# Performance work log

Measured on AMD Instinct MI355X. Metric: run time of the kernel, lower is better.

The kernel has to match this reference:

```python
import jax, jax.numpy as jnp
import numpy as np

N = 100000
E = 600000
IN_DIM = 128
HID = 128


def setup_inputs() -> dict:
    key = jax.random.key(0)
    ks = jax.random.split(key, 12)
    def lin(kw, fan_in, fan_out):
        # torch nn.Linear default init: U(-1/sqrt(fan_in), 1/sqrt(fan_in))
        bound = 1.0 / np.sqrt(fan_in)
        kw1, kw2 = jax.random.split(kw)
        w = jax.random.uniform(kw1, (fan_in, fan_out), jnp.float32, -bound, bound)
        b = jax.random.uniform(kw2, (fan_out,), jnp.float32, -bound, bound)
        return w, b
    x = jax.random.normal(ks[0], (N, IN_DIM), jnp.float32)
    edge_index = jax.random.randint(ks[1], (2, E), 0, N, jnp.int64)
    w1a, b1a = lin(ks[2], IN_DIM, HID)
    w1b, b1b = lin(ks[3], HID, HID)
    w2a, b2a = lin(ks[4], HID, HID)
    w2b, b2b = lin(ks[5], HID, HID)
    wo, bo = lin(ks[6], HID, 1)
    return {"x": x, "edge_index": edge_index,
            "w1a": w1a, "b1a": b1a, "w1b": w1b, "b1b": b1b,
            "w2a": w2a, "b2a": b2a, "w2b": w2b, "b2b": b2b,
            "wo": wo, "bo": bo}


def _gin_conv(x, src, dst, wa, ba, wb, bb):
    # sum-aggregate neighbor features: agg[dst] += x[src]; eps = 0 (GIN default)
    agg = jax.ops.segment_sum(x[src], dst, num_segments=N)
    h = x + agg
    h = jax.nn.relu(h @ wa + ba)
    return h @ wb + bb


def reference(x, edge_index, w1a, b1a, w1b, b1b, w2a, b2a, w2b, b2b, wo, bo):
    src, dst = edge_index[0], edge_index[1]
    h = _gin_conv(x, src, dst, w1a, b1a, w1b, b1b)
    h = _gin_conv(h, src, dst, w2a, b2a, w2b, b2b)
    return (h @ wo + bo).squeeze(-1)  # [N]
```

## Files before the change

### kernel.cpp

```cpp
#include <hip/hip_runtime.h>

typedef unsigned short u16;
typedef unsigned int u32;
typedef __bf16 bf16x8 __attribute__((ext_vector_type(8)));
typedef float f32x4 __attribute__((ext_vector_type(4)));

#define CAP 32

__device__ __forceinline__ u16 f2bf(float f) {
  union { float f; u32 u; } c; c.f = f;
  return (u16)((c.u + 0x7fffu + ((c.u >> 16) & 1u)) >> 16);
}
__device__ __forceinline__ float2 upk2(u32 v) {
  union { u32 u; float f; } a, b; a.u = v << 16; b.u = v & 0xffff0000u;
  return make_float2(a.f, b.f);
}
__device__ __forceinline__ u32 pk2(float x, float y) {
  return (u32)f2bf(x) | ((u32)f2bf(y) << 16);
}

__global__ __launch_bounds__(256) void k_prep2(const float4* __restrict__ x4,
                                               uint2* __restrict__ xb,
                                               int n4, int castBlocks, int trBlocks,
                                               const float* __restrict__ w0,
                                               const float* __restrict__ w1,
                                               const float* __restrict__ w2,
                                               const float* __restrict__ w3,
                                               u16* __restrict__ wT,
                                               int* __restrict__ cursor, int N) {
  int b = blockIdx.x, t = threadIdx.x;
  if (b < castBlocks) {
    int i = b * 256 + t;
    if (i < n4) {
      float4 v = x4[i];
      xb[i] = make_uint2(pk2(v.x, v.y), pk2(v.z, v.w));
    }
  } else if (b < castBlocks + trBlocks) {
    int id = (b - castBlocks) * 256 + t;
    int w = id >> 14, rem = id & 16383;
    int nn = rem >> 7, kk = rem & 127;
    const float* s = (w == 0) ? w0 : (w == 1) ? w1 : (w == 2) ? w2 : w3;
    wT[id] = f2bf(s[kk * 128 + nn]);
  } else {
    int i = (b - castBlocks - trBlocks) * 256 + t;
    if (i < N) cursor[i] = 0;
  }
}

__global__ __launch_bounds__(256) void k_fillp(const int* __restrict__ src,
                                               const int* __restrict__ dst,
                                               int* __restrict__ cursor,
                                               int* __restrict__ edge_src, int E) {
  int e = blockIdx.x * 256 + threadIdx.x;
  if (e < E) {
    int d = dst[e];
    int pos = atomicAdd(&cursor[d], 1);
    if (pos < CAP) edge_src[d * CAP + pos] = src[e];
  }
}

__global__ __launch_bounds__(256) void k_agg(const uint4* __restrict__ in,
                                             uint4* __restrict__ out,
                                             const int* __restrict__ cursor,
                                             const int* __restrict__ edge_src, int N) {
  int node = __builtin_amdgcn_readfirstlane(blockIdx.x * 4 + (threadIdx.x >> 6));
  if (node >= N) return;
  int lane = threadIdx.x & 63;
  int g = lane >> 4, l = lane & 15;

  int myedge = edge_src[node * CAP + (lane & 31)];
  int cnt = cursor[node];
  uint4 sv = in[(size_t)node * 16 + l];

  float acc[8];
#pragma unroll
  for (int i = 0; i < 8; ++i) acc[i] = 0.f;

  auto fma8 = [&](uint4 v, float w) {
    float2 p;
    p = upk2(v.x); acc[0] = fmaf(w, p.x, acc[0]); acc[1] = fmaf(w, p.y, acc[1]);
    p = upk2(v.y); acc[2] = fmaf(w, p.x, acc[2]); acc[3] = fmaf(w, p.y, acc[3]);
    p = upk2(v.z); acc[4] = fmaf(w, p.x, acc[4]); acc[5] = fmaf(w, p.y, acc[5]);
    p = upk2(v.w); acc[6] = fmaf(w, p.x, acc[6]); acc[7] = fmaf(w, p.y, acc[7]);
  };

  fma8(sv, (g == 0) ? 1.f : 0.f);
  cnt = (cnt < CAP) ? cnt : CAP;

  for (int b = 0; b < cnt; b += 8) {
    int sa = b + g, sb = b + 4 + g;
    int ia = __shfl(myedge, sa & 31, 64);
    int ib = __shfl(myedge, sb & 31, 64);
    bool aa = sa < cnt, ab = sb < cnt;
    int pa = aa ? ia : node;
    int pb = ab ? ib : node;
    uint4 va = in[(size_t)pa * 16 + l];
    uint4 vb = in[(size_t)pb * 16 + l];
    fma8(va, aa ? 1.f : 0.f);
    fma8(vb, ab ? 1.f : 0.f);
  }

#pragma unroll
  for (int i = 0; i < 8; ++i) {
    acc[i] += __shfl_xor(acc[i], 16, 64);
    acc[i] += __shfl_xor(acc[i], 32, 64);
  }
  if (g == 0) {
    uint4 o;
    o.x = pk2(acc[0], acc[1]);
    o.y = pk2(acc[2], acc[3]);
    o.z = pk2(acc[4], acc[5]);
    o.w = pk2(acc[6], acc[7]);
    out[(size_t)node * 16 + l] = o;
  }
}

template <bool HEAD>
__global__ __launch_bounds__(256) void k_mlp(const u16* __restrict__ in,
                                             const u16* __restrict__ wAT,
                                             const float* __restrict__ bA,
                                             const u16* __restrict__ wBT,
                                             const float* __restrict__ bB,
                                             const float* __restrict__ wo,
                                             const float* __restrict__ bo,
                                             void* __restrict__ outp,
                                             int N, int ntiles) {
  __shared__ u16 lA[64 * 128];
  __shared__ u16 lW[2 * 128 * 128];
  const int tid = threadIdx.x;
  const int wave = tid >> 6, lane = tid & 63;
  const int m16 = lane & 15, quad = lane >> 4;

#pragma unroll
  for (int it = 0; it < 16; ++it) {
    int id = it * 256 + tid;
    int m = id >> 11, rem = id & 2047;
    int row = rem >> 4, c = rem & 15;
    const u16* s = m ? wBT : wAT;
    uint4 v = *(const uint4*)&s[row * 128 + c * 8];
    *(uint4*)&lW[m * 16384 + row * 128 + ((c ^ (row & 15)) << 3)] = v;
  }

  float bAr[8], bBr[8], woR[8], bBh[8];
#pragma unroll
  for (int t = 0; t < 8; ++t) {
    bAr[t] = bA[t * 16 + m16];
    bBr[t] = HEAD ? 0.f : bB[t * 16 + m16];
    woR[t] = HEAD ? wo[t * 16 + m16] : 0.f;
    bBh[t] = HEAD ? bB[t * 16 + m16] : 0.f;
  }
  float boV = HEAD ? bo[0] : 0.f;

  __syncthreads();

  const int mrow = wave * 16 + m16;

  uint4 pf[4];
  auto gload = [&](int tl) {
#pragma unroll
    for (int it = 0; it < 4; ++it) {
      int gr = tl * 64 + wave * 16 + it * 4 + quad;
      uint4 v = make_uint4(0u, 0u, 0u, 0u);
      if (gr < N) v = *(const uint4*)&in[(size_t)gr * 128 + m16 * 8];
      pf[it] = v;
    }
  };

  int tile = blockIdx.x;
  if (tile < ntiles) gload(tile);
  for (; tile < ntiles; tile += gridDim.x) {
#pragma unroll
    for (int it = 0; it < 4; ++it) {
      int row = wave * 16 + it * 4 + quad;
      *(uint4*)&lA[row * 128 + ((m16 ^ (row & 15)) << 3)] = pf[it];
    }
    bf16x8 aF[4];
#pragma unroll
    for (int ks = 0; ks < 4; ++ks)
      aF[ks] = *(const bf16x8*)&lA[mrow * 128 + (((ks * 4 + quad) ^ m16) << 3)];
    int nxt = tile + gridDim.x;
    if (nxt < ntiles) gload(nxt);

    f32x4 acc[8];
#pragma unroll
    for (int t = 0; t < 8; ++t) acc[t] = (f32x4){0.f, 0.f, 0.f, 0.f};
#pragma unroll
    for (int t = 0; t < 8; ++t) {
      int nrow = t * 16 + m16;
#pragma unroll
      for (int ks = 0; ks < 4; ++ks) {
        bf16x8 bF = *(const bf16x8*)&lW[nrow * 128 + (((ks * 4 + quad) ^ m16) << 3)];
        acc[t] = __builtin_amdgcn_mfma_f32_16x16x32_bf16(aF[ks], bF, acc[t], 0, 0, 0);
      }
    }
#pragma unroll
    for (int t = 0; t < 8; ++t) {
      int n = t * 16 + m16;
#pragma unroll
      for (int r = 0; r < 4; ++r) {
        int rloc = quad * 4 + r;
        int absrow = wave * 16 + rloc;
        float v = acc[t][r] + bAr[t];
        v = v > 0.f ? v : 0.f;
        lA[absrow * 128 + ((((n >> 3) ^ rloc) << 3) | (n & 7))] = f2bf(v);
      }
    }
#pragma unroll
    for (int ks = 0; ks < 4; ++ks)
      aF[ks] = *(const bf16x8*)&lA[mrow * 128 + (((ks * 4 + quad) ^ m16) << 3)];
#pragma unroll
    for (int t = 0; t < 8; ++t) acc[t] = (f32x4){0.f, 0.f, 0.f, 0.f};
#pragma unroll
    for (int t = 0; t < 8; ++t) {
      int nrow = t * 16 + m16;
#pragma unroll
      for (int ks = 0; ks < 4; ++ks) {
        bf16x8 bF = *(const bf16x8*)&lW[16384 + nrow * 128 + (((ks * 4 + quad) ^ m16) << 3)];
        acc[t] = __builtin_amdgcn_mfma_f32_16x16x32_bf16(aF[ks], bF, acc[t], 0, 0, 0);
      }
    }
    if (!HEAD) {
#pragma unroll
      for (int t = 0; t < 8; ++t) {
        int n = t * 16 + m16;
#pragma unroll
        for (int r = 0; r < 4; ++r) {
          int rloc = quad * 4 + r;
          int absrow = wave * 16 + rloc;
          float v = acc[t][r] + bBr[t];
          lA[absrow * 128 + ((((n >> 3) ^ rloc) << 3) | (n & 7))] = f2bf(v);
        }
      }
      u16* out = (u16*)outp;
#pragma unroll
      for (int it = 0; it < 4; ++it) {
        int row = wave * 16 + it * 4 + quad;
        int gr = tile * 64 + row;
        if (gr < N) {
          uint4 v = *(const uint4*)&lA[row * 128 + ((m16 ^ (row & 15)) << 3)];
          *(uint4*)&out[(size_t)gr * 128 + m16 * 8] = v;
        }
      }
    } else {
      float* out = (float*)outp;
      float s[4];
#pragma unroll
      for (int r = 0; r < 4; ++r) {
        float v = 0.f;
#pragma unroll
        for (int t = 0; t < 8; ++t) v += (acc[t][r] + bBh[t]) * woR[t];
        s[r] = v;
      }
#pragma unroll
      for (int r = 0; r < 4; ++r) {
        s[r] += __shfl_xor(s[r], 1, 64);
        s[r] += __shfl_xor(s[r], 2, 64);
        s[r] += __shfl_xor(s[r], 4, 64);
        s[r] += __shfl_xor(s[r], 8, 64);
      }
      if (m16 == 0) {
#pragma unroll
        for (int r = 0; r < 4; ++r) {
          int gr = tile * 64 + wave * 16 + quad * 4 + r;
          if (gr < N) out[gr] = s[r] + boV;
        }
      }
    }
  }
}

extern "C" void kernel_launch(void* const* d_in, const int* in_sizes, int n_in,
                              void* d_out, int out_size, void* d_ws, size_t ws_size,
                              hipStream_t stream) {
  const float* x = (const float*)d_in[0];
  const int* ei = (const int*)d_in[1];
  const int E = in_sizes[1] / 2;
  const int N = in_sizes[0] / 128;
  const int* srcI = ei;
  const int* dstI = ei + E;
  const float* w1a = (const float*)d_in[2];
  const float* b1a = (const float*)d_in[3];
  const float* w1b = (const float*)d_in[4];
  const float* b1b = (const float*)d_in[5];
  const float* w2a = (const float*)d_in[6];
  const float* b2a = (const float*)d_in[7];
  const float* w2b = (const float*)d_in[8];
  const float* b2b = (const float*)d_in[9];
  const float* wo = (const float*)d_in[10];
  const float* bo = (const float*)d_in[11];

  char* ws = (char*)d_ws;
  size_t off = 0;
  auto nx = [&](size_t bytes) {
    size_t o = off;
    off += (bytes + 511) & ~(size_t)511;
    return o;
  };
  int* cursor   = (int*)(ws + nx((size_t)N * 4));
  int* edge_src = (int*)(ws + nx((size_t)N * CAP * 4));
  u16* wT       = (u16*)(ws + nx((size_t)4 * 16384 * 2));
  u16* xb       = (u16*)(ws + nx((size_t)N * 128 * 2));
  u16* bufA     = (u16*)(ws + nx((size_t)N * 128 * 2));
  u16* bufB     = (u16*)(ws + nx((size_t)N * 128 * 2));

  const int n4 = N * 32;
  const int castBlocks = (n4 + 255) / 256;
  const int trBlocks = 256;
  const int zeroBlocks = (N + 255) / 256;

  k_prep2<<<castBlocks + trBlocks + zeroBlocks, 256, 0, stream>>>(
      (const float4*)x, (uint2*)xb, n4, castBlocks, trBlocks,
      w1a, w1b, w2a, w2b, wT, cursor, N);
  k_fillp<<<(E + 255) / 256, 256, 0, stream>>>(srcI, dstI, cursor, edge_src, E);

  const int aggBlocks = (N + 3) / 4;
  const int ntiles = (N + 63) / 64;
  const int mlpGrid = 512;

  k_agg<<<aggBlocks, 256, 0, stream>>>((const uint4*)xb, (uint4*)bufA, cursor, edge_src, N);
  k_mlp<false><<<mlpGrid, 256, 0, stream>>>(bufA, wT, b1a, wT + 16384, b1b,
                                            nullptr, nullptr, bufB, N, ntiles);
  k_agg<<<aggBlocks, 256, 0, stream>>>((const uint4*)bufB, (uint4*)xb, cursor, edge_src, N);
  k_mlp<true><<<mlpGrid, 256, 0, stream>>>(xb, wT + 32768, b2a, wT + 49152, b2b,
                                           wo, bo, d_out, N, ntiles);
}
```

Before: 234.7 us.

## Assign four nodes per wavefront in aggregation, one per 16-lane group

The aggregation kernel now gives each 16-lane group its own destination node instead of splitting one node's edges across four groups. This removes the cross-group shuffle reduction and the idle masked lanes. Each group loads its neighbor indices as int2 and issues eight neighbor row loads per iteration for more memory-level parallelism. Lane groups in a wave now loop a different number of times when degrees differ, so some lanes sit idle; the grid shrinks fourfold to match.

```diff
diff --git a/kernel.cpp b/kernel.cpp
--- a/kernel.cpp
+++ b/kernel.cpp
@@ -63,14 +63,19 @@
                                              uint4* __restrict__ out,
                                              const int* __restrict__ cursor,
                                              const int* __restrict__ edge_src, int N) {
-  int node = __builtin_amdgcn_readfirstlane(blockIdx.x * 4 + (threadIdx.x >> 6));
-  if (node >= N) return;
   int lane = threadIdx.x & 63;
   int g = lane >> 4, l = lane & 15;
-
-  int myedge = edge_src[node * CAP + (lane & 31)];
-  int cnt = cursor[node];
-  uint4 sv = in[(size_t)node * 16 + l];
+  int wid = blockIdx.x * 4 + (threadIdx.x >> 6);
+  int node = wid * 4 + g;
+  bool valid = node < N;
+  int nc = valid ? node : (N - 1);
+
+  int2 e = *(const int2*)&edge_src[nc * CAP + 2 * l];
+  int cnt = cursor[nc];
+  uint4 sv = in[(size_t)nc * 16 + l];
+
+  cnt = valid ? cnt : 0;
+  cnt = (cnt < CAP) ? cnt : CAP;
 
   float acc[8];
 #pragma unroll
@@ -84,28 +89,22 @@
     p = upk2(v.w); acc[6] = fmaf(w, p.x, acc[6]); acc[7] = fmaf(w, p.y, acc[7]);
   };
 
-  fma8(sv, (g == 0) ? 1.f : 0.f);
-  cnt = (cnt < CAP) ? cnt : CAP;
+  fma8(sv, 1.f);
 
   for (int b = 0; b < cnt; b += 8) {
-    int sa = b + g, sb = b + 4 + g;
-    int ia = __shfl(myedge, sa & 31, 64);
-    int ib = __shfl(myedge, sb & 31, 64);
-    bool aa = sa < cnt, ab = sb < cnt;
-    int pa = aa ? ia : node;
-    int pb = ab ? ib : node;
-    uint4 va = in[(size_t)pa * 16 + l];
-    uint4 vb = in[(size_t)pb * 16 + l];
-    fma8(va, aa ? 1.f : 0.f);
-    fma8(vb, ab ? 1.f : 0.f);
-  }
-
-#pragma unroll
-  for (int i = 0; i < 8; ++i) {
-    acc[i] += __shfl_xor(acc[i], 16, 64);
-    acc[i] += __shfl_xor(acc[i], 32, 64);
-  }
-  if (g == 0) {
+    uint4 v[8];
+#pragma unroll
+    for (int k = 0; k < 8; ++k) {
+      int idx = __shfl((k & 1) ? e.y : e.x, (g << 4) + (b >> 1) + (k >> 1), 64);
+      bool act = (b + k) < cnt;
+      int p = act ? idx : nc;
+      v[k] = in[(size_t)p * 16 + l];
+    }
+#pragma unroll
+    for (int k = 0; k < 8; ++k) fma8(v[k], ((b + k) < cnt) ? 1.f : 0.f);
+  }
+
+  if (valid) {
     uint4 o;
     o.x = pk2(acc[0], acc[1]);
     o.y = pk2(acc[2], acc[3]);
@@ -313,7 +312,7 @@
       w1a, w1b, w2a, w2b, wT, cursor, N);
   k_fillp<<<(E + 255) / 256, 256, 0, stream>>>(srcI, dstI, cursor, edge_src, E);
 
-  const int aggBlocks = (N + 3) / 4;
+  const int aggBlocks = (N + 15) / 16;
   const int ntiles = (N + 63) / 64;
   const int mlpGrid = 512;
 
```

After: 234.1 us. About the same (-0.2%).
